# Optimization experiments

Measured on AMD Instinct MI355X. Metric: run time of the kernel, lower is better.

The kernel has to match this reference:

```python
import jax, jax.numpy as jnp
import numpy as np

S, B, D, H, MLP_H, W = 2048, 4, 1024, 16, 4096, 16
EPS = 1e-6

def _ln(x):
    m = jnp.mean(x, axis=-1, keepdims=True)
    v = jnp.var(x, axis=-1, keepdims=True)
    return (x - m) / jnp.sqrt(v + EPS)

def setup_inputs() -> dict:
    key = jax.random.key(0)
    ks = jax.random.split(key, 12)
    sc = lambda k, shape, fan: jax.random.normal(k, shape, jnp.float32) / np.sqrt(fan)
    return {
        'x': jax.random.normal(ks[0], (S, B, D), jnp.float32),
        'c': jax.random.normal(ks[1], (B, D), jnp.float32),
        'ada_w': sc(ks[2], (6 * D, D), D),
        'ada_b': jax.random.normal(ks[3], (6 * D,), jnp.float32) * 0.02,
        'in_proj_w': sc(ks[4], (3 * D, D), D),
        'in_proj_b': jax.random.normal(ks[5], (3 * D,), jnp.float32) * 0.02,
        'out_proj_w': sc(ks[6], (D, D), D),
        'out_proj_b': jax.random.normal(ks[7], (D,), jnp.float32) * 0.02,
        'mlp_w1': sc(ks[8], (MLP_H, D), D),
        'mlp_b1': jax.random.normal(ks[9], (MLP_H,), jnp.float32) * 0.02,
        'mlp_w2': sc(ks[10], (D, MLP_H), MLP_H),
        'mlp_b2': jax.random.normal(ks[11], (D,), jnp.float32) * 0.02,
        'num_heads': H,
        'window_size': W,
    }

def _attn(x, in_proj_w, in_proj_b, out_proj_w, out_proj_b, num_heads, window_size):
    s, b, d = x.shape
    dh = d // num_heads
    qkv = x @ in_proj_w.T + in_proj_b            # [S,B,3D]
    q, k, v = jnp.split(qkv, 3, axis=-1)
    def heads(t):  # [S,B,D] -> [B,H,S,dh]
        return t.reshape(s, b, num_heads, dh).transpose(1, 2, 0, 3)
    q, k, v = heads(q), heads(k), heads(v)
    scores = jnp.einsum('bhsd,bhtd->bhst', q, k) / np.sqrt(dh)
    idx = jnp.arange(s)
    band = jnp.abs(idx[:, None] - idx[None, :]) <= window_size  # [S,S]
    scores = jnp.where(band[None, None], scores, -jnp.inf)
    attn = jax.nn.softmax(scores, axis=-1)
    o = jnp.einsum('bhst,bhtd->bhsd', attn, v)   # [B,H,S,dh]
    o = o.transpose(2, 0, 1, 3).reshape(s, b, d)
    return o @ out_proj_w.T + out_proj_b

def reference(x, c, ada_w, ada_b, in_proj_w, in_proj_b, out_proj_w, out_proj_b, mlp_w1, mlp_b1, mlp_w2, mlp_b2, num_heads, window_size):
    mod = jax.nn.relu(c) @ ada_w.T + ada_b       # [B,6D]
    sh_msa, sc_msa, g_msa, sh_mlp, sc_mlp, g_mlp = jnp.split(mod, 6, axis=1)
    xm = _ln(x) * (1.0 + sc_msa[None]) + sh_msa[None]
    x = x + g_msa[None] * _attn(xm, in_proj_w, in_proj_b, out_proj_w, out_proj_b, num_heads, window_size)
    xm = _ln(x) * (1.0 + sc_mlp[None]) + sh_mlp[None]
    h = jax.nn.relu(xm @ mlp_w1.T + mlp_b1)
    mlp_out = h @ mlp_w2.T + mlp_b2
    return x + g_mlp[None] * mlp_out
```

## Files before the change

### kernel.cpp

```cpp
#include <hip/hip_runtime.h>

#define S_LEN 2048
#define BATCH 4
#define DMODEL 1024
#define NHEAD 16
#define MROWS (S_LEN * BATCH)
#define MOD6 (6 * DMODEL)

typedef float f32x4 __attribute__((ext_vector_type(4)));
typedef short bf16x8 __attribute__((ext_vector_type(8)));
typedef unsigned short ushort_t;

__device__ __forceinline__ unsigned short f2bf(float f) {
  unsigned u = __float_as_uint(f);
  u += 0x7FFF + ((u >> 16) & 1);
  return (unsigned short)(u >> 16);
}
__device__ __forceinline__ float bf2f(unsigned short h) {
  return __uint_as_float(((unsigned)h) << 16);
}
__device__ __forceinline__ float wave_sum(float v) {
#pragma unroll
  for (int off = 32; off > 0; off >>= 1) v += __shfl_xor(v, off, 64);
  return v;
}
__device__ __forceinline__ void mfma16(f32x4& c, bf16x8 a, bf16x8 b) {
  asm volatile("v_mfma_f32_16x16x32_bf16 %0, %1, %2, %0" : "+v"(c) : "v"(a), "v"(b));
}
__device__ __forceinline__ void mfma_fence() {
  __builtin_amdgcn_sched_barrier(0);
  asm volatile("s_nop 7\n\ts_nop 7\n\ts_nop 7");
  __builtin_amdgcn_sched_barrier(0);
}
__device__ __forceinline__ void async16(const void* g, void* l) {
  __builtin_amdgcn_global_load_lds((const __attribute__((address_space(1))) void*)g,
                                   (__attribute__((address_space(3))) void*)l, 16, 0, 0);
}

__launch_bounds__(256)
__global__ void castk(const float4* __restrict__ in, ushort4* __restrict__ out, int n4) {
  int i = blockIdx.x * 256 + threadIdx.x;
  if (i < n4) {
    float4 v = in[i];
    ushort4 o;
    o.x = f2bf(v.x); o.y = f2bf(v.y); o.z = f2bf(v.z); o.w = f2bf(v.w);
    out[i] = o;
  }
}

__launch_bounds__(256)
__global__ void ada_k(const float* __restrict__ c, const float* __restrict__ aw,
                      const float* __restrict__ ab, float* __restrict__ mod) {
  int j = blockIdx.x;
  int b = threadIdx.x >> 6;
  int l = threadIdx.x & 63;
  const float* wrow = aw + (size_t)j * DMODEL;
  const float* crow = c + b * DMODEL;
  float s = 0.f;
#pragma unroll 4
  for (int i = l; i < DMODEL; i += 64) {
    float cv = crow[i];
    cv = cv > 0.f ? cv : 0.f;
    s += cv * wrow[i];
  }
  s = wave_sum(s);
  if (l == 0) mod[b * MOD6 + j] = s + ab[j];
}

__launch_bounds__(256)
__global__ void ln_mod(const float* __restrict__ x, const float* __restrict__ mod,
                       int sh_off, int sc_off, ushort_t* __restrict__ out) {
  __shared__ float red[8];
  int row = blockIdx.x;
  int b = row & 3;
  int tid = threadIdx.x;
  const float4* xr = (const float4*)(x + (size_t)row * DMODEL);
  float4 v = xr[tid];
  float s = v.x + v.y + v.z + v.w;
  float s2 = v.x * v.x + v.y * v.y + v.z * v.z + v.w * v.w;
  s = wave_sum(s);
  s2 = wave_sum(s2);
  int w = tid >> 6, l = tid & 63;
  if (l == 0) { red[w] = s; red[4 + w] = s2; }
  __syncthreads();
  s = red[0] + red[1] + red[2] + red[3];
  s2 = red[4] + red[5] + red[6] + red[7];
  float mean = s * (1.0f / DMODEL);
  float var = s2 * (1.0f / DMODEL) - mean * mean;
  float inv = rsqrtf(var + 1e-6f);
  const float* shp = mod + b * MOD6 + sh_off;
  const float* scp = mod + b * MOD6 + sc_off;
  float vv[4] = {v.x, v.y, v.z, v.w};
  ushort4 ov;
  ushort_t* op = (ushort_t*)&ov;
#pragma unroll
  for (int j = 0; j < 4; j++) {
    int idx = tid * 4 + j;
    float y = (vv[j] - mean) * inv * (1.0f + scp[idx]) + shp[idx];
    op[j] = f2bf(y);
  }
  ((ushort4*)(out + (size_t)row * DMODEL))[tid] = ov;
}

__launch_bounds__(256)
__global__ void attn_mfma(const ushort_t* __restrict__ qkv, ushort_t* __restrict__ out) {
  const int l = threadIdx.x & 63;
  const int widx = blockIdx.x * 4 + (threadIdx.x >> 6);
  const int qblk = widx & 63;
  const int bh = widx >> 6;
  const int h = bh & 15;
  const int b = bh >> 4;
  const int q0 = qblk * 32;
  int k0 = q0 - 16;
  if (k0 < 0) k0 = 0;
  if (k0 > S_LEN - 64) k0 = S_LEN - 64;
  const int lr = l & 15;
  const int g = l >> 4;

  const char* base = (const char*)qkv;

  bf16x8 qf[2][2], kf[4][2];
#pragma unroll
  for (int nt = 0; nt < 2; nt++) {
    size_t rowb = (size_t)((q0 + 16 * nt + lr) * 4 + b) * 6144 + h * 128 + 16 * g;
#pragma unroll
    for (int ks = 0; ks < 2; ks++)
      qf[nt][ks] = *(const bf16x8*)(base + rowb + 64 * ks);
  }
#pragma unroll
  for (int mt = 0; mt < 4; mt++) {
    size_t rowb = (size_t)((k0 + 16 * mt + lr) * 4 + b) * 6144 + 2048 + h * 128 + 16 * g;
#pragma unroll
    for (int ks = 0; ks < 2; ks++)
      kf[mt][ks] = *(const bf16x8*)(base + rowb + 64 * ks);
  }

  f32x4 acc[4][2] = {};
#pragma unroll
  for (int mt = 0; mt < 4; mt++)
#pragma unroll
    for (int nt = 0; nt < 2; nt++)
#pragma unroll
      for (int ks = 0; ks < 2; ks++)
        mfma16(acc[mt][nt], kf[mt][ks], qf[nt][ks]);
  mfma_fence();

  float p0[16], p1[16];
  const int sq0 = q0 + lr, sq1 = q0 + 16 + lr;
  float m0 = -1e30f, m1 = -1e30f;
#pragma unroll
  for (int mt = 0; mt < 4; mt++)
#pragma unroll
    for (int i = 0; i < 4; i++) {
      int sk = k0 + 16 * mt + 4 * g + i;
      int d0 = sq0 - sk, d1 = sq1 - sk;
      float s0 = (d0 <= 16 && d0 >= -16) ? acc[mt][0][i] * 0.125f : -1e30f;
      float s1 = (d1 <= 16 && d1 >= -16) ? acc[mt][1][i] * 0.125f : -1e30f;
      p0[mt * 4 + i] = s0;
      p1[mt * 4 + i] = s1;
      m0 = fmaxf(m0, s0);
      m1 = fmaxf(m1, s1);
    }
  m0 = fmaxf(m0, __shfl_xor(m0, 16, 64));
  m0 = fmaxf(m0, __shfl_xor(m0, 32, 64));
  m1 = fmaxf(m1, __shfl_xor(m1, 16, 64));
  m1 = fmaxf(m1, __shfl_xor(m1, 32, 64));
  float l0 = 0.f, l1 = 0.f;
#pragma unroll
  for (int j = 0; j < 16; j++) {
    float e0 = __expf(p0[j] - m0);
    float e1 = __expf(p1[j] - m1);
    p0[j] = e0; p1[j] = e1;
    l0 += e0; l1 += e1;
  }
  l0 += __shfl_xor(l0, 16, 64); l0 += __shfl_xor(l0, 32, 64);
  l1 += __shfl_xor(l1, 16, 64); l1 += __shfl_xor(l1, 32, 64);
  const float inv0 = 1.0f / l0, inv1 = 1.0f / l1;

  const size_t vb = (size_t)b * 6144 + 4096 + h * 128;
  for (int c = 0; c < 8; c++) {
    float o0[8] = {}, o1[8] = {};
#pragma unroll
    for (int mt = 0; mt < 4; mt++)
#pragma unroll
      for (int i = 0; i < 4; i++) {
        int t = k0 + 16 * mt + 4 * g + i;
        bf16x8 v = *(const bf16x8*)(base + (size_t)t * 24576 + vb + 16 * c);
        float pa = p0[mt * 4 + i], pb = p1[mt * 4 + i];
#pragma unroll
        for (int d = 0; d < 8; d++) {
          float vf = bf2f((unsigned short)v[d]);
          o0[d] += pa * vf;
          o1[d] += pb * vf;
        }
      }
#pragma unroll
    for (int d = 0; d < 8; d++) {
      o0[d] += __shfl_xor(o0[d], 16, 64); o0[d] += __shfl_xor(o0[d], 32, 64);
      o1[d] += __shfl_xor(o1[d], 16, 64); o1[d] += __shfl_xor(o1[d], 32, 64);
    }
    if (g < 2) {
      int sq = q0 + 16 * g + lr;
      bf16x8 ov;
#pragma unroll
      for (int d = 0; d < 8; d++) {
        float val = (g ? o1[d] : o0[d]) * (g ? inv1 : inv0);
        ov[d] = (short)f2bf(val);
      }
      *(bf16x8*)((char*)out + (size_t)(sq * 4 + b) * 2048 + h * 128 + c * 16) = ov;
    }
  }
}

template <int EPI>
__launch_bounds__(256)
__global__ void gemm_bt(const ushort_t* __restrict__ A, const ushort_t* __restrict__ W,
                        const float* __restrict__ bias, const float* __restrict__ res,
                        const float* __restrict__ gmod, void* __restrict__ outp,
                        int M, int N, int K) {
  __shared__ alignas(16) ushort_t As[128 * 32];
  __shared__ alignas(16) ushort_t Bs[128 * 32];
  const int tid = threadIdx.x;
  const int w = tid >> 6;
  const int l = tid & 63;
  const int row0 = blockIdx.y * 128;
  const int col0 = blockIdx.x * 128;
  const int wr = (w >> 1) * 64;
  const int wc = (w & 1) * 64;

  f32x4 acc[4][4] = {};

  const int rr = tid >> 2;
  const int cc = (tid & 3) << 3;
  const ushort_t* ga = A + (size_t)(row0 + rr) * K + cc;
  const ushort_t* gb = W + (size_t)(col0 + rr) * K + cc;
  char* lA = (char*)As + w * 1024;
  char* lB = (char*)Bs + w * 1024;

  const int lrow = l & 15;
  const int lko = (l >> 4) * 16;
  const char* Ard = (const char*)As + (wr + lrow) * 64 + lko;
  const char* Brd = (const char*)Bs + (wc + lrow) * 64 + lko;

  for (int k0 = 0; k0 < K; k0 += 32) {
    async16(ga, lA);
    async16(ga + 64 * (size_t)K, lA + 4096);
    async16(gb, lB);
    async16(gb + 64 * (size_t)K, lB + 4096);
    ga += 32;
    gb += 32;
    __syncthreads();
    bf16x8 afr[4], bfr[4];
#pragma unroll
    for (int m = 0; m < 4; m++) afr[m] = *(const bf16x8*)(Ard + m * 16 * 64);
#pragma unroll
    for (int n = 0; n < 4; n++) bfr[n] = *(const bf16x8*)(Brd + n * 16 * 64);
#pragma unroll
    for (int m = 0; m < 4; m++)
#pragma unroll
      for (int n = 0; n < 4; n++) mfma16(acc[m][n], afr[m], bfr[n]);
    __syncthreads();
  }
  mfma_fence();

  const int crow = row0 + wr + (l >> 4) * 4;
  const int ccol = col0 + wc + lrow;
#pragma unroll
  for (int m = 0; m < 4; m++) {
#pragma unroll
    for (int i = 0; i < 4; i++) {
      int grow = crow + m * 16 + i;
#pragma unroll
      for (int n = 0; n < 4; n++) {
        int gcol = ccol + n * 16;
        float v = acc[m][n][i] + bias[gcol];
        if constexpr (EPI == 0) {
          ((ushort_t*)outp)[(size_t)grow * N + gcol] = f2bf(v);
        } else if constexpr (EPI == 1) {
          ((ushort_t*)outp)[(size_t)grow * N + gcol] = f2bf(v > 0.f ? v : 0.f);
        } else {
          int bb = grow & 3;
          ((float*)outp)[(size_t)grow * N + gcol] =
              res[(size_t)grow * N + gcol] + gmod[bb * MOD6 + gcol] * v;
        }
      }
    }
  }
}

extern "C" void kernel_launch(void* const* d_in, const int* in_sizes, int n_in,
                              void* d_out, int out_size, void* d_ws, size_t ws_size,
                              hipStream_t stream) {
  const float* x     = (const float*)d_in[0];
  const float* c     = (const float*)d_in[1];
  const float* ada_w = (const float*)d_in[2];
  const float* ada_b = (const float*)d_in[3];
  const float* in_w  = (const float*)d_in[4];
  const float* in_b  = (const float*)d_in[5];
  const float* out_w = (const float*)d_in[6];
  const float* out_b = (const float*)d_in[7];
  const float* w1    = (const float*)d_in[8];
  const float* b1    = (const float*)d_in[9];
  const float* w2    = (const float*)d_in[10];
  const float* b2    = (const float*)d_in[11];

  char* ws = (char*)d_ws;
  float* mod    = (float*)ws;
  ushort_t* wq  = (ushort_t*)(ws + 98304);
  ushort_t* wo  = (ushort_t*)(ws + 6389760);
  ushort_t* wm1 = (ushort_t*)(ws + 8486912);
  ushort_t* wm2 = (ushort_t*)(ws + 16875520);
  ushort_t* xm  = (ushort_t*)(ws + 25264128);
  ushort_t* qkv = (ushort_t*)(ws + 42041344);
  ushort_t* att = (ushort_t*)(ws + 92372992);
  ushort_t* h   = (ushort_t*)(ws + 42041344);
  float* x1 = (float*)d_out;

  castk<<<(3072 * 1024 / 4 + 255) / 256, 256, 0, stream>>>((const float4*)in_w, (ushort4*)wq, 3072 * 1024 / 4);
  castk<<<(1024 * 1024 / 4 + 255) / 256, 256, 0, stream>>>((const float4*)out_w, (ushort4*)wo, 1024 * 1024 / 4);
  castk<<<(4096 * 1024 / 4 + 255) / 256, 256, 0, stream>>>((const float4*)w1, (ushort4*)wm1, 4096 * 1024 / 4);
  castk<<<(1024 * 4096 / 4 + 255) / 256, 256, 0, stream>>>((const float4*)w2, (ushort4*)wm2, 1024 * 4096 / 4);

  ada_k<<<MOD6, 256, 0, stream>>>(c, ada_w, ada_b, mod);

  ln_mod<<<MROWS, 256, 0, stream>>>(x, mod, 0, 1024, xm);
  gemm_bt<0><<<dim3(3072 / 128, MROWS / 128), 256, 0, stream>>>(xm, wq, in_b, nullptr, nullptr, qkv, MROWS, 3072, 1024);
  attn_mfma<<<(BATCH * NHEAD * (S_LEN / 32)) / 4, 256, 0, stream>>>(qkv, att);
  gemm_bt<2><<<dim3(1024 / 128, MROWS / 128), 256, 0, stream>>>(att, wo, out_b, x, mod + 2 * DMODEL, x1, MROWS, 1024, 1024);
  ln_mod<<<MROWS, 256, 0, stream>>>(x1, mod, 3 * DMODEL, 4 * DMODEL, xm);
  gemm_bt<1><<<dim3(4096 / 128, MROWS / 128), 256, 0, stream>>>(xm, wm1, b1, nullptr, nullptr, h, MROWS, 4096, 1024);
  gemm_bt<2><<<dim3(1024 / 128, MROWS / 128), 256, 0, stream>>>(h, wm2, b2, x1, mod + 5 * DMODEL, (float*)d_out, MROWS, 1024, 4096);
}
```

Measured before the change: 368.4 us.

## Double-buffer GEMM LDS tiles and XOR-swizzle k-chunks to cut bank conflicts

The bf16 GEMM now keeps two LDS buffers for the A and B tiles. It issues the async global-to-LDS copy of the next K-slice before the MFMAs on the current one, and drops one barrier per iteration. It also permutes the 16-byte k-chunks within each row by XOR with the row index, applied on both the load side and the fragment read side, to reduce LDS bank conflicts on the fragment reads. This doubles LDS use per block, which may lower occupancy. How much overlap it actually gets depends on whether the barrier forces a wait for all outstanding loads.

```diff
diff --git a/kernel.cpp b/kernel.cpp
--- a/kernel.cpp
+++ b/kernel.cpp
@@ -218,8 +218,8 @@
                         const float* __restrict__ bias, const float* __restrict__ res,
                         const float* __restrict__ gmod, void* __restrict__ outp,
                         int M, int N, int K) {
-  __shared__ alignas(16) ushort_t As[128 * 32];
-  __shared__ alignas(16) ushort_t Bs[128 * 32];
+  __shared__ alignas(16) ushort_t As[2][128 * 32];
+  __shared__ alignas(16) ushort_t Bs[2][128 * 32];
   const int tid = threadIdx.x;
   const int w = tid >> 6;
   const int l = tid & 63;
@@ -231,25 +231,42 @@
   f32x4 acc[4][4] = {};
 
   const int rr = tid >> 2;
-  const int cc = (tid & 3) << 3;
+  const int cc = (((tid & 3) ^ (rr & 3)) << 3);
   const ushort_t* ga = A + (size_t)(row0 + rr) * K + cc;
   const ushort_t* gb = W + (size_t)(col0 + rr) * K + cc;
-  char* lA = (char*)As + w * 1024;
-  char* lB = (char*)Bs + w * 1024;
+  const int ldst = w * 1024;
 
   const int lrow = l & 15;
-  const int lko = (l >> 4) * 16;
-  const char* Ard = (const char*)As + (wr + lrow) * 64 + lko;
-  const char* Brd = (const char*)Bs + (wc + lrow) * 64 + lko;
-
-  for (int k0 = 0; k0 < K; k0 += 32) {
+  const int g = l >> 4;
+  const int aoff = (wr + lrow) * 64 + ((g ^ (lrow & 3)) << 4);
+  const int boff = (wc + lrow) * 64 + ((g ^ (lrow & 3)) << 4);
+
+  const int nk = K >> 5;
+  int cur = 0;
+  {
+    char* lA = (char*)As[0] + ldst;
+    char* lB = (char*)Bs[0] + ldst;
     async16(ga, lA);
     async16(ga + 64 * (size_t)K, lA + 4096);
     async16(gb, lB);
     async16(gb + 64 * (size_t)K, lB + 4096);
     ga += 32;
     gb += 32;
+  }
+  for (int it = 0; it < nk; ++it) {
     __syncthreads();
+    if (it + 1 < nk) {
+      char* lA = (char*)As[cur ^ 1] + ldst;
+      char* lB = (char*)Bs[cur ^ 1] + ldst;
+      async16(ga, lA);
+      async16(ga + 64 * (size_t)K, lA + 4096);
+      async16(gb, lB);
+      async16(gb + 64 * (size_t)K, lB + 4096);
+      ga += 32;
+      gb += 32;
+    }
+    const char* Ard = (const char*)As[cur] + aoff;
+    const char* Brd = (const char*)Bs[cur] + boff;
     bf16x8 afr[4], bfr[4];
 #pragma unroll
     for (int m = 0; m < 4; m++) afr[m] = *(const bf16x8*)(Ard + m * 16 * 64);
@@ -259,7 +276,7 @@
     for (int m = 0; m < 4; m++)
 #pragma unroll
       for (int n = 0; n < 4; n++) mfma16(acc[m][n], afr[m], bfr[n]);
-    __syncthreads();
+    cur ^= 1;
   }
   mfma_fence();
 
```

Measured after the change: 381.6 us. 1.04x slower.

## Double GEMM K-tile to 64 with XOR-swizzled LDS layout

Applied to the files above, without the earlier changes.

The bf16 GEMM now stages a 64-wide K slice per iteration instead of 32, which halves the number of barrier pairs and loop iterations. The LDS layout uses an XOR swizzle on 16-byte chunks keyed by row, so fragment reads from the 128-byte rows avoid bank conflicts. LDS use doubles to 32 KB per block, which may lower occupancy, and there is still no double buffering, so loads and MFMAs still do not overlap.

```diff
diff --git a/kernel.cpp b/kernel.cpp
--- a/kernel.cpp
+++ b/kernel.cpp
@@ -218,8 +218,8 @@
                         const float* __restrict__ bias, const float* __restrict__ res,
                         const float* __restrict__ gmod, void* __restrict__ outp,
                         int M, int N, int K) {
-  __shared__ alignas(16) ushort_t As[128 * 32];
-  __shared__ alignas(16) ushort_t Bs[128 * 32];
+  __shared__ alignas(16) ushort_t As[128 * 64];
+  __shared__ alignas(16) ushort_t Bs[128 * 64];
   const int tid = threadIdx.x;
   const int w = tid >> 6;
   const int l = tid & 63;
@@ -230,40 +230,47 @@
 
   f32x4 acc[4][4] = {};
 
-  const int rr = tid >> 2;
-  const int cc = (tid & 3) << 3;
-  const ushort_t* ga = A + (size_t)(row0 + rr) * K + cc;
-  const ushort_t* gb = W + (size_t)(col0 + rr) * K + cc;
+  const int srow = tid >> 3;
+  const int scc = (((tid & 7) ^ (srow & 7)) << 3);
+  const ushort_t* ga = A + (size_t)(row0 + srow) * K + scc;
+  const ushort_t* gb = W + (size_t)(col0 + srow) * K + scc;
   char* lA = (char*)As + w * 1024;
   char* lB = (char*)Bs + w * 1024;
 
   const int lrow = l & 15;
-  const int lko = (l >> 4) * 16;
-  const char* Ard = (const char*)As + (wr + lrow) * 64 + lko;
-  const char* Brd = (const char*)Bs + (wc + lrow) * 64 + lko;
-
-  for (int k0 = 0; k0 < K; k0 += 32) {
-    async16(ga, lA);
-    async16(ga + 64 * (size_t)K, lA + 4096);
-    async16(gb, lB);
-    async16(gb + 64 * (size_t)K, lB + 4096);
-    ga += 32;
-    gb += 32;
+  const int g = l >> 4;
+  const int cx0 = ((g ^ (lrow & 7)) << 4);
+  const int cx1 = (((4 + g) ^ (lrow & 7)) << 4);
+  const int arow = (wr + lrow) * 128;
+  const int brow = (wc + lrow) * 128;
+
+  const int nk = K >> 6;
+  for (int it = 0; it < nk; ++it) {
+#pragma unroll
+    for (int r = 0; r < 4; r++) async16(ga + (size_t)(32 * r) * K, lA + r * 4096);
+#pragma unroll
+    for (int r = 0; r < 4; r++) async16(gb + (size_t)(32 * r) * K, lB + r * 4096);
+    ga += 64;
+    gb += 64;
     __syncthreads();
-    bf16x8 afr[4], bfr[4];
-#pragma unroll
-    for (int m = 0; m < 4; m++) afr[m] = *(const bf16x8*)(Ard + m * 16 * 64);
-#pragma unroll
-    for (int n = 0; n < 4; n++) bfr[n] = *(const bf16x8*)(Brd + n * 16 * 64);
-#pragma unroll
-    for (int m = 0; m < 4; m++)
-#pragma unroll
-      for (int n = 0; n < 4; n++) mfma16(acc[m][n], afr[m], bfr[n]);
+#pragma unroll
+    for (int kk = 0; kk < 2; kk++) {
+      const int cx = kk ? cx1 : cx0;
+      bf16x8 afr[4], bfr[4];
+#pragma unroll
+      for (int m = 0; m < 4; m++) afr[m] = *(const bf16x8*)((char*)As + arow + m * 2048 + cx);
+#pragma unroll
+      for (int n = 0; n < 4; n++) bfr[n] = *(const bf16x8*)((char*)Bs + brow + n * 2048 + cx);
+#pragma unroll
+      for (int m = 0; m < 4; m++)
+#pragma unroll
+        for (int n = 0; n < 4; n++) mfma16(acc[m][n], afr[m], bfr[n]);
+    }
     __syncthreads();
   }
   mfma_fence();
 
-  const int crow = row0 + wr + (l >> 4) * 4;
+  const int crow = row0 + wr + g * 4;
   const int ccol = col0 + wc + lrow;
 #pragma unroll
   for (int m = 0; m < 4; m++) {
```

Result: faster. 328.6 us (-10.8%).
